# Kernel tuning notes

Hardware: AMD Instinct MI355X
Metric: run time of the kernel (lower is better)

The kernel has to match this reference:

```python
import jax, jax.numpy as jnp
import numpy as np

B, C, O, N, T, K = 4, 64, 64, 32768, 4, 9
PAD, DIL = 4, 1  # padding*dilation, dilation
SIGMA = 0.05
EPS_BN = 1e-5


def _gather_ch(x, idx):
    # x: [B, C, N], idx: [B, N] -> gather along last dim per channel
    idx3 = jnp.broadcast_to(idx[:, None, :], x.shape)
    return jnp.take_along_axis(x, idx3, axis=-1)


def _weighted_conv(x, coords, w):
    # x: [B,C,N], coords: [B,3,N], w: [O,C,K]
    xp = jnp.pad(x, ((0, 0), (0, 0), (PAD, PAD)))
    cp = jnp.pad(coords, ((0, 0), (0, 0), (PAD, PAD)))
    win_idx = jnp.arange(N)[:, None] + jnp.arange(K) * DIL  # [N, K]
    win = xp[:, :, win_idx]   # [B,C,N,K]
    cwin = cp[:, :, win_idx]  # [B,3,N,K]
    d = cwin - cwin[:, :, :, K // 2:K // 2 + 1]
    s = jnp.sum(d * d, axis=1)                    # [B,N,K]
    r = jnp.sqrt(jnp.where(s > 0, s, 1.0))
    r = jnp.where(s > 0, r, 0.0)
    wgt = jnp.maximum(1.0 - r / SIGMA, 0.0)       # [B,N,K]
    return jnp.einsum('bcnk,bnk,ock->bon', win, wgt, w)


def _bn(x, g, b):
    # training-mode BatchNorm1d over (B, N)
    m = jnp.mean(x, axis=(0, 2), keepdims=True)
    v = jnp.var(x, axis=(0, 2), keepdims=True)
    return g[None, :, None] * (x - m) * jax.lax.rsqrt(v + EPS_BN) + b[None, :, None]


def setup_inputs() -> dict:
    key = jax.random.key(0)
    ks = jax.random.split(key, 12)
    inp = jax.random.normal(ks[0], (B, C, N), dtype=jnp.float32)
    # coords in a small box so sigma=0.05 yields non-trivial weights
    multi_coords = jax.random.uniform(ks[1], (B, 3, N, T), dtype=jnp.float32) * 0.02
    indices = jax.random.randint(ks[2], (B, N, T), 0, N, dtype=jnp.int32)
    reindices = jax.random.randint(ks[3], (B, N, T), 0, N, dtype=jnp.int32)
    fan = C * K
    conv_w = jax.random.normal(ks[4], (T, O, C, K), dtype=jnp.float32) / np.sqrt(fan)
    bn_gamma = jnp.ones((T, O), dtype=jnp.float32)
    bn_beta = jnp.zeros((T, O), dtype=jnp.float32)
    fusion_w = jax.random.normal(ks[5], (O, T * O), dtype=jnp.float32) / np.sqrt(T * O)
    fusion_b = jnp.zeros((O,), dtype=jnp.float32)
    fusion_gamma = jnp.ones((O,), dtype=jnp.float32)
    fusion_beta = jnp.zeros((O,), dtype=jnp.float32)
    return {"input": inp, "multi_coords": multi_coords, "indices": indices,
            "reindices": reindices, "conv_w": conv_w, "bn_gamma": bn_gamma,
            "bn_beta": bn_beta, "fusion_w": fusion_w, "fusion_b": fusion_b,
            "fusion_gamma": fusion_gamma, "fusion_beta": fusion_beta}


def reference(input, multi_coords, indices, reindices, conv_w, bn_gamma, bn_beta,
              fusion_w, fusion_b, fusion_gamma, fusion_beta):
    outs = []
    for i in range(T):  # fixed small set of 4 Hilbert orders
        x = _gather_ch(input, indices[:, :, i])            # [B,C,N]
        x = _weighted_conv(x, multi_coords[:, :, :, i], conv_w[i])  # [B,O,N]
        x = _bn(x, bn_gamma[i], bn_beta[i])
        x = _gather_ch(x, reindices[:, :, i])
        outs.append(x)
    cat = jnp.concatenate(outs, axis=1)                    # [B, T*O, N]
    y = jnp.einsum('bcn,oc->bon', cat, fusion_w) + fusion_b[None, :, None]
    y = _bn(y, fusion_gamma, fusion_beta)
    return jax.nn.relu(y)
```

## Files before the change

### kernel.cpp

```cpp
#include <hip/hip_runtime.h>
#include <hip/hip_bf16.h>

#define BB 4
#define CC 64
#define OO 64
#define NN 32768
#define TT 4
#define KK 9
#define PADW 4
#define SIGMA 0.05f
#define EPS_BN 1e-5f

typedef __attribute__((ext_vector_type(8))) short bf16x8;
typedef __attribute__((ext_vector_type(4))) float f32x4;

__device__ __forceinline__ unsigned short f2bf(float f) {
  __hip_bfloat16 h = __float2bfloat16(f);
  return *reinterpret_cast<unsigned short*>(&h);
}
__device__ __forceinline__ unsigned int pkbf(float a, float b) {
  float2 t; t.x = a; t.y = b;
  __hip_bfloat162 h = __float22bfloat162_rn(t);
  unsigned int r;
  __builtin_memcpy(&r, &h, 4);
  return r;
}

__global__ __launch_bounds__(256) void prep_kernel(
    const float* __restrict__ inp, unsigned short* __restrict__ xTb,
    const float* __restrict__ cw,  unsigned short* __restrict__ W4,
    const int*   __restrict__ ind, const float* __restrict__ mc,
    int* __restrict__ indT, float* __restrict__ mcT)
{
  __shared__ float xt[64][65];
  const int bid = blockIdx.x;
  const int tid = threadIdx.x;

  if (bid < 2048) {
    const int n0 = (bid & 511) * 64;
    const int b  = bid >> 9;
    {
      int nl = tid & 63, c4 = tid >> 6;
      #pragma unroll
      for (int i = 0; i < 16; ++i) {
        int c = c4 * 16 + i;
        xt[c][nl] = inp[((size_t)(b*CC + c))*NN + n0 + nl];
      }
    }
    __syncthreads();
    {
      int nl = tid >> 2, cq = tid & 3;
      unsigned int pk[8];
      #pragma unroll
      for (int i = 0; i < 8; ++i) {
        int c = cq*16 + i*2;
        pk[i] = pkbf(xt[c][nl], xt[c+1][nl]);
      }
      unsigned int* dst = (unsigned int*)(xTb + (((size_t)b*NN) + n0 + nl)*CC + cq*16);
      ((int4*)dst)[0] = make_int4((int)pk[0],(int)pk[1],(int)pk[2],(int)pk[3]);
      ((int4*)dst)[1] = make_int4((int)pk[4],(int)pk[5],(int)pk[6],(int)pk[7]);
    }
  } else if (bid < 2560) {
    const int id = bid - 2048;
    const int n  = (id & 127) * 256 + tid;
    const int b  = id >> 7;
    int4 iv = *(const int4*)(ind + ((size_t)b*NN + n)*TT);
    indT[((size_t)(0*BB + b))*NN + n] = iv.x;
    indT[((size_t)(1*BB + b))*NN + n] = iv.y;
    indT[((size_t)(2*BB + b))*NN + n] = iv.z;
    indT[((size_t)(3*BB + b))*NN + n] = iv.w;
    #pragma unroll
    for (int d = 0; d < 3; ++d) {
      float4 mv = *(const float4*)(mc + (((size_t)(b*3 + d))*NN + n)*TT);
      mcT[((size_t)((0*BB + b)*3 + d))*NN + n] = mv.x;
      mcT[((size_t)((1*BB + b)*3 + d))*NN + n] = mv.y;
      mcT[((size_t)((2*BB + b)*3 + d))*NN + n] = mv.z;
      mcT[((size_t)((3*BB + b)*3 + d))*NN + n] = mv.w;
    }
  } else {
    const int id = bid - 2560;
    const int k = id % KK;
    const int t = id / KK;
    for (int u = tid; u < OO*CC; u += 256) {
      int o = u >> 6, c = u & 63;
      int ow = o >> 5, ot = (o >> 4) & 1, l15 = o & 15;
      int frag = c >> 5, q = (c >> 3) & 3, j = c & 7;
      float wv = cw[(((size_t)(t*OO + o))*CC + c)*KK + k];
      W4[(size_t)(t*9+k)*4096 + ow*2048 + ot*1024 + frag*512 + l15*32 + q*8 + j]
          = f2bf(wv);
    }
  }
}

__global__ __launch_bounds__(256, 3) void conv_kernel(
    const unsigned short* __restrict__ xTb,
    const float* __restrict__ mcT,
    const int*   __restrict__ indT,
    const unsigned short* __restrict__ W4,
    unsigned short* __restrict__ Y,
    float* __restrict__ cpart2)
{
  const int n0  = blockIdx.x * 256;
  const int b   = blockIdx.y;
  const int t   = blockIdx.z;
  const int tid = threadIdx.x;
  const int lane = tid & 63;
  const int w    = tid >> 6;
  const int l15  = lane & 15;
  const int q    = lane >> 4;
  const int ow   = w & 1;
  const int nw   = w >> 1;

  __shared__ short xg[264*64];
  __shared__ float wgl[256][10];
  __shared__ float mcs[3][268];
  __shared__ int   ids[268];

  for (int u = tid; u < 264; u += 256) {
    int m = n0 + u - PADW;
    bool v = (m >= 0) && (m < NN);
    ids[u] = v ? indT[((size_t)(t*BB + b))*NN + m] : -1;
    #pragma unroll
    for (int d = 0; d < 3; ++d)
      mcs[d][u] = v ? mcT[((size_t)((t*BB + b)*3 + d))*NN + m] : 0.f;
  }
  __syncthreads();

  int4 g[9];
  #pragma unroll
  for (int i = 0; i < 9; ++i) {
    int u = tid + 256*i;
    g[i] = make_int4(0,0,0,0);
    if (u < 2112) {
      int p = u >> 3, s = u & 7;
      int idx = ids[p];
      if (idx >= 0)
        g[i] = *(const int4*)(xTb + ((size_t)b*NN + idx)*CC + s*8);
    }
  }

  {
    int nl = tid;
    float cx = mcs[0][nl+4], cy = mcs[1][nl+4], cz = mcs[2][nl+4];
    #pragma unroll
    for (int k = 0; k < KK; ++k) {
      float dx = mcs[0][nl+k]-cx, dy = mcs[1][nl+k]-cy, dz = mcs[2][nl+k]-cz;
      float s2 = dx*dx + dy*dy + dz*dz;
      float r = (s2 > 0.f) ? sqrtf(s2) : 0.f;
      wgl[nl][k] = fmaxf(1.f - r*(1.f/SIGMA), 0.f);
    }
  }

  #pragma unroll
  for (int i = 0; i < 9; ++i) {
    int u = tid + 256*i;
    if (u < 2112) {
      int p = u >> 3, s = u & 7;
      *(int4*)&xg[(p << 6) + ((s ^ (p & 7)) << 3)] = g[i];
    }
  }
  __syncthreads();

  const unsigned short* Wt = W4 + (size_t)t*9*4096 + ow*2048 + (l15*4 + q)*8;
  const f32x4 Z = {0.f, 0.f, 0.f, 0.f};
  f32x4 fin[2][8];
  #pragma unroll
  for (int ot = 0; ot < 2; ++ot)
    #pragma unroll
    for (int ns = 0; ns < 8; ++ns) fin[ot][ns] = Z;

  for (int k = 0; k < KK; ++k) {
    const unsigned short* Wk = Wt + (size_t)k*4096;
    bf16x8 af[2][2];
    #pragma unroll
    for (int ot = 0; ot < 2; ++ot) {
      af[ot][0] = *(const bf16x8*)(Wk + ot*1024);
      af[ot][1] = *(const bf16x8*)(Wk + ot*1024 + 512);
    }
    #pragma unroll
    for (int ns = 0; ns < 8; ++ns) {
      int nl = nw*128 + ns*16 + l15;
      int p  = nl + k;
      const short* row = &xg[p << 6];
      int sw = p & 7;
      bf16x8 b0 = *(const bf16x8*)(row + ((q ^ sw) << 3));
      bf16x8 b1 = *(const bf16x8*)(row + (((4 + q) ^ sw) << 3));
      float wgt = wgl[nl][k];
      #pragma unroll
      for (int ot = 0; ot < 2; ++ot) {
        f32x4 d = __builtin_amdgcn_mfma_f32_16x16x32_bf16(af[ot][0], b0, Z, 0, 0, 0);
        d = __builtin_amdgcn_mfma_f32_16x16x32_bf16(af[ot][1], b1, d, 0, 0, 0);
        fin[ot][ns] += wgt * d;
      }
    }
  }

  #pragma unroll
  for (int ns = 0; ns < 8; ++ns) {
    int nl = nw*128 + ns*16 + l15;
    size_t row = (((size_t)t*BB + b)*NN + n0 + nl)*OO;
    #pragma unroll
    for (int ot = 0; ot < 2; ++ot) {
      uint2 pk2;
      pk2.x = pkbf(fin[ot][ns][0], fin[ot][ns][1]);
      pk2.y = pkbf(fin[ot][ns][2], fin[ot][ns][3]);
      *(uint2*)(Y + row + ow*32 + ot*16 + q*4) = pk2;
    }
  }

  float sv[16];
  #pragma unroll
  for (int ot = 0; ot < 2; ++ot)
    #pragma unroll
    for (int r = 0; r < 4; ++r) {
      float a = 0.f, qs = 0.f;
      #pragma unroll
      for (int ns = 0; ns < 8; ++ns) {
        float v = fin[ot][ns][r];
        a += v; qs += v*v;
      }
      sv[ot*4+r] = a; sv[8+ot*4+r] = qs;
    }
  #pragma unroll
  for (int msk = 1; msk < 16; msk <<= 1) {
    #pragma unroll
    for (int i = 0; i < 16; ++i) sv[i] += __shfl_xor(sv[i], msk, 16);
  }
  if (l15 == 0) {
    int slot4 = ((b*128 + (int)blockIdx.x) << 2) | w;
    #pragma unroll
    for (int ot = 0; ot < 2; ++ot)
      #pragma unroll
      for (int r = 0; r < 4; ++r) {
        int o = ow*32 + ot*16 + q*4 + r;
        cpart2[((size_t)((t*64 + o)*2 + 0))*2048 + slot4] = sv[ot*4+r];
        cpart2[((size_t)((t*64 + o)*2 + 1))*2048 + slot4] = sv[8+ot*4+r];
      }
  }
}

__global__ __launch_bounds__(256) void bnparam_kernel(
    const float* __restrict__ cpart2,
    const float* __restrict__ gam,
    const float* __restrict__ bet,
    float* __restrict__ ss)
{
  const int to = blockIdx.x;
  const int tid = threadIdx.x;
  __shared__ float r1[256], r2[256];
  const float* p1 = cpart2 + (size_t)to*2*2048;
  const float* p2 = p1 + 2048;
  float s1 = 0.f, s2 = 0.f;
  for (int i = tid*4; i < 2048; i += 1024) {
    float4 a = *(const float4*)(p1 + i);
    float4 c = *(const float4*)(p2 + i);
    s1 += a.x + a.y + a.z + a.w;
    s2 += c.x + c.y + c.z + c.w;
  }
  r1[tid] = s1; r2[tid] = s2;
  __syncthreads();
  for (int st = 128; st > 0; st >>= 1) {
    if (tid < st) { r1[tid] += r1[tid+st]; r2[tid] += r2[tid+st]; }
    __syncthreads();
  }
  if (tid == 0) {
    const float inv = 1.f / (float)(BB * NN);
    float mean = r1[0] * inv;
    float var  = r2[0] * inv - mean * mean;
    float sc = gam[to] * rsqrtf(var + EPS_BN);
    ss[to*2 + 0] = sc;
    ss[to*2 + 1] = bet[to] - mean * sc;
  }
}

__global__ __launch_bounds__(256) void wfuse_kernel(
    const float* __restrict__ fw,
    const float* __restrict__ fb,
    const float* __restrict__ ss,
    float* __restrict__ fbp,
    unsigned short* __restrict__ FWB)
{
  const int tid = threadIdx.x;
  {
    int o = tid >> 2, c0 = (tid & 3) * 64;
    float s = 0.f;
    for (int c = c0; c < c0 + 64; ++c)
      s += fw[o*256 + c] * ss[c*2 + 1];
    s += __shfl_xor(s, 1);
    s += __shfl_xor(s, 2);
    if ((tid & 3) == 0) fbp[o] = fb[o] + s;
  }
  for (int e = tid; e < 16384; e += 256) {
    int rk  = e >> 11;
    int ow  = (e >> 10) & 1;
    int ot  = (e >> 9) & 1;
    int l15 = (e >> 5) & 15;
    int cj  = e & 31;
    int o = ow*32 + ot*16 + l15;
    int c = (rk >> 1)*64 + (rk & 1)*32 + cj;
    FWB[e] = f2bf(fw[o*256 + c] * ss[c*2]);
  }
}

__global__ __launch_bounds__(256, 4) void fusion_kernel(
    const unsigned short* __restrict__ Y,
    const int*   __restrict__ rind,
    const unsigned short* __restrict__ FWB,
    const float* __restrict__ fbp,
    float* __restrict__ out,
    float* __restrict__ fpart2)
{
  const int n0  = blockIdx.x * 128;
  const int b   = blockIdx.y;
  const int tid = threadIdx.x;
  const int lane = tid & 63;
  const int w    = tid >> 6;
  const int l15  = lane & 15;
  const int q    = lane >> 4;
  const int ow   = w & 1;
  const int nw   = w >> 1;

  __shared__ short zg[128*64];

  int4 rg[4];
  #pragma unroll
  for (int i = 0; i < 4; ++i) {
    int n = (tid >> 3) + 32*i;
    rg[i] = *(const int4*)(rind + ((size_t)b*NN + n0 + n)*TT);
  }

  f32x4 fin[2][4];
  #pragma unroll
  for (int ot = 0; ot < 2; ++ot)
    #pragma unroll
    for (int ns = 0; ns < 4; ++ns) fin[ot][ns] = (f32x4){0.f,0.f,0.f,0.f};

  #pragma unroll
  for (int r = 0; r < 4; ++r) {
    if (r) __syncthreads();
    #pragma unroll
    for (int i = 0; i < 4; ++i) {
      int u = tid + 256*i;
      int n = u >> 3, s = u & 7;
      int rn = (r == 0) ? rg[i].x : (r == 1) ? rg[i].y
             : (r == 2) ? rg[i].z : rg[i].w;
      int4 raw = *(const int4*)(Y + (((size_t)r*BB + b)*NN + rn)*OO + s*8);
      *(int4*)&zg[(n << 6) + ((s ^ (n & 7)) << 3)] = raw;
    }
    __syncthreads();

    #pragma unroll
    for (int kk = 0; kk < 2; ++kk) {
      int rk = r*2 + kk;
      const unsigned short* wp = FWB + rk*2048 + ow*1024 + (l15*4 + q)*8;
      bf16x8 af[2];
      af[0] = *(const bf16x8*)(wp);
      af[1] = *(const bf16x8*)(wp + 512);
      #pragma unroll
      for (int ns = 0; ns < 4; ++ns) {
        int nl = nw*64 + ns*16 + l15;
        int ch = (kk*4 + q) ^ (nl & 7);
        bf16x8 bfr = *(const bf16x8*)&zg[(nl << 6) + (ch << 3)];
        #pragma unroll
        for (int ot = 0; ot < 2; ++ot)
          fin[ot][ns] = __builtin_amdgcn_mfma_f32_16x16x32_bf16(af[ot], bfr, fin[ot][ns], 0, 0, 0);
      }
    }
  }

  float sv[16];
  #pragma unroll
  for (int ot = 0; ot < 2; ++ot)
    #pragma unroll
    for (int r2 = 0; r2 < 4; ++r2) {
      int o = ow*32 + ot*16 + q*4 + r2;
      float bias = fbp[o];
      float* dst = out + ((size_t)(b*OO + o))*NN + n0 + nw*64;
      float a = 0.f, qs = 0.f;
      #pragma unroll
      for (int ns = 0; ns < 4; ++ns) {
        float v = fin[ot][ns][r2] + bias;
        dst[ns*16 + l15] = v;
        a += v; qs += v*v;
      }
      sv[ot*4+r2] = a; sv[8+ot*4+r2] = qs;
    }
  #pragma unroll
  for (int msk = 1; msk < 16; msk <<= 1) {
    #pragma unroll
    for (int i = 0; i < 16; ++i) sv[i] += __shfl_xor(sv[i], msk, 16);
  }
  if (l15 == 0) {
    int slot4 = ((b*256 + (int)blockIdx.x) << 2) | w;
    #pragma unroll
    for (int ot = 0; ot < 2; ++ot)
      #pragma unroll
      for (int r2 = 0; r2 < 4; ++r2) {
        int o = ow*32 + ot*16 + q*4 + r2;
        fpart2[((size_t)(o*2 + 0))*4096 + slot4] = sv[ot*4+r2];
        fpart2[((size_t)(o*2 + 1))*4096 + slot4] = sv[8+ot*4+r2];
      }
  }
}

__global__ __launch_bounds__(256) void freduce_kernel(
    const float* __restrict__ fpart2,
    const float* __restrict__ fg,
    const float* __restrict__ fbeta,
    float* __restrict__ fss)
{
  const int o = blockIdx.x;
  const int tid = threadIdx.x;
  __shared__ float r1[256], r2[256];
  const float* p1 = fpart2 + (size_t)o*2*4096;
  const float* p2 = p1 + 4096;
  float s1 = 0.f, s2 = 0.f;
  for (int i = tid*4; i < 4096; i += 1024) {
    float4 a = *(const float4*)(p1 + i);
    float4 c = *(const float4*)(p2 + i);
    s1 += a.x + a.y + a.z + a.w;
    s2 += c.x + c.y + c.z + c.w;
  }
  r1[tid] = s1; r2[tid] = s2;
  __syncthreads();
  for (int st = 128; st > 0; st >>= 1) {
    if (tid < st) { r1[tid] += r1[tid+st]; r2[tid] += r2[tid+st]; }
    __syncthreads();
  }
  if (tid == 0) {
    const float inv = 1.f / (float)(BB * NN);
    float mean = r1[0] * inv;
    float var  = r2[0] * inv - mean * mean;
    float sc = fg[o] * rsqrtf(var + EPS_BN);
    fss[o*2 + 0] = sc;
    fss[o*2 + 1] = fbeta[o] - mean * sc;
  }
}

__global__ __launch_bounds__(256) void final_kernel(
    float* __restrict__ out, const float* __restrict__ fss)
{
  const int e0 = blockIdx.x * 2048 + threadIdx.x;
  #pragma unroll
  for (int s = 0; s < 8; ++s) {
    int e  = e0 + s * 256;
    int o2 = (e >> 15) & 63;
    float sc = fss[o2*2 + 0];
    float sh = fss[o2*2 + 1];
    float v = out[e] * sc + sh;
    out[e] = fmaxf(v, 0.f);
  }
}

extern "C" void kernel_launch(void* const* d_in, const int* in_sizes, int n_in,
                              void* d_out, int out_size, void* d_ws, size_t ws_size,
                              hipStream_t stream) {
  const float* inp  = (const float*)d_in[0];
  const float* mc   = (const float*)d_in[1];
  const int*   ind  = (const int*)  d_in[2];
  const int*   rind = (const int*)  d_in[3];
  const float* cw   = (const float*)d_in[4];
  const float* bg   = (const float*)d_in[5];
  const float* bb   = (const float*)d_in[6];
  const float* fw   = (const float*)d_in[7];
  const float* fb   = (const float*)d_in[8];
  const float* fg   = (const float*)d_in[9];
  const float* fbt  = (const float*)d_in[10];

  char* ws = (char*)d_ws;
  float* convss = (float*)(ws + 0);
  float* fss    = (float*)(ws + 2048);
  float* fbp    = (float*)(ws + 3072);
  unsigned short* Y = (unsigned short*)(ws + 8192);
  float* fpart2 = (float*)(ws + 8192 + 67108864);
  unsigned short* FWB = (unsigned short*)(ws + 8192 + 67108864 + 2097152);

  char* ob = (char*)d_out;
  unsigned short* xTb = (unsigned short*)ob;
  unsigned short* W4  = (unsigned short*)(ob + 16777216);
  float* cpart2 = (float*)(ob + 17072128);
  int*   indT   = (int*)  (ob + 21266432);
  float* mcT    = (float*)(ob + 23363584);
  float* out = (float*)d_out;

  prep_kernel<<<2596, 256, 0, stream>>>(inp, xTb, cw, W4, ind, mc, indT, mcT);

  dim3 gc(NN/256, BB, TT);
  conv_kernel<<<gc, 256, 0, stream>>>(xTb, mcT, indT, W4, Y, cpart2);

  bnparam_kernel<<<256, 256, 0, stream>>>(cpart2, bg, bb, convss);

  wfuse_kernel<<<1, 256, 0, stream>>>(fw, fb, convss, fbp, FWB);

  dim3 gf(NN/128, BB);
  fusion_kernel<<<gf, 256, 0, stream>>>(Y, rind, FWB, fbp, out, fpart2);

  freduce_kernel<<<OO, 256, 0, stream>>>(fpart2, fg, fbt, fss);

  final_kernel<<<(BB*OO*NN)/2048, 256, 0, stream>>>(out, fss);
}
```

Measured before the change: 216.2 us.

## Use direct global-to-LDS loads for gathers in conv and fusion kernels

Replaces the register-staged gather (global load into registers, then swizzled LDS store) in the conv and fusion kernels with global_load_lds 16-byte direct copies. The swizzle moves to the source address, and a zeroed page in workspace stands in for out-of-range rows. The fusion kernel also hoists its weight fragment loads ahead of the barrier, and the final ReLU/BN kernel switches to float4 accesses. This is meant to cut VGPR pressure and LDS write instructions and to overlap gathers with the weight computation, at the cost of relying on the per-wave contiguous LDS layout of global_load_lds.

Measured after the change: 220.6 us. 1.02x slower.

```diff
diff --git a/kernel.cpp b/kernel.cpp
--- a/kernel.cpp
+++ b/kernel.cpp
@@ -25,12 +25,19 @@
   __builtin_memcpy(&r, &h, 4);
   return r;
 }
+__device__ __forceinline__ void gload16(const void* g, void* l) {
+  __builtin_amdgcn_global_load_lds(
+      (const __attribute__((address_space(1))) void*)g,
+      (__attribute__((address_space(3))) void*)l,
+      16, 0, 0);
+}
 
 __global__ __launch_bounds__(256) void prep_kernel(
     const float* __restrict__ inp, unsigned short* __restrict__ xTb,
     const float* __restrict__ cw,  unsigned short* __restrict__ W4,
     const int*   __restrict__ ind, const float* __restrict__ mc,
-    int* __restrict__ indT, float* __restrict__ mcT)
+    int* __restrict__ indT, float* __restrict__ mcT,
+    float* __restrict__ zpage)
 {
   __shared__ float xt[64][65];
   const int bid = blockIdx.x;
@@ -77,7 +84,7 @@
       mcT[((size_t)((2*BB + b)*3 + d))*NN + n] = mv.z;
       mcT[((size_t)((3*BB + b)*3 + d))*NN + n] = mv.w;
     }
-  } else {
+  } else if (bid < 2596) {
     const int id = bid - 2560;
     const int k = id % KK;
     const int t = id / KK;
@@ -89,6 +96,8 @@
       W4[(size_t)(t*9+k)*4096 + ow*2048 + ot*1024 + frag*512 + l15*32 + q*8 + j]
           = f2bf(wv);
     }
+  } else {
+    zpage[tid] = 0.f;
   }
 }
 
@@ -97,6 +106,7 @@
     const float* __restrict__ mcT,
     const int*   __restrict__ indT,
     const unsigned short* __restrict__ W4,
+    const float* __restrict__ zpage,
     unsigned short* __restrict__ Y,
     float* __restrict__ cpart2)
 {
@@ -126,16 +136,18 @@
   }
   __syncthreads();
 
-  int4 g[9];
   #pragma unroll
   for (int i = 0; i < 9; ++i) {
-    int u = tid + 256*i;
-    g[i] = make_int4(0,0,0,0);
-    if (u < 2112) {
-      int p = u >> 3, s = u & 7;
+    int chunk = w + 4*i;
+    if (chunk < 33) {
+      int u = chunk*64 + lane;
+      int p = u >> 3, c = u & 7;
       int idx = ids[p];
-      if (idx >= 0)
-        g[i] = *(const int4*)(xTb + ((size_t)b*NN + idx)*CC + s*8);
+      int sg = c ^ (p & 7);
+      const void* src = (idx >= 0)
+          ? (const void*)(xTb + ((size_t)b*NN + idx)*CC + sg*8)
+          : (const void*)((const unsigned short*)zpage + c*8);
+      gload16(src, &xg[chunk*512]);
     }
   }
 
@@ -148,15 +160,6 @@
       float s2 = dx*dx + dy*dy + dz*dz;
       float r = (s2 > 0.f) ? sqrtf(s2) : 0.f;
       wgl[nl][k] = fmaxf(1.f - r*(1.f/SIGMA), 0.f);
-    }
-  }
-
-  #pragma unroll
-  for (int i = 0; i < 9; ++i) {
-    int u = tid + 256*i;
-    if (u < 2112) {
-      int p = u >> 3, s = u & 7;
-      *(int4*)&xg[(p << 6) + ((s ^ (p & 7)) << 3)] = g[i];
     }
   }
   __syncthreads();
@@ -340,22 +343,25 @@
     if (r) __syncthreads();
     #pragma unroll
     for (int i = 0; i < 4; ++i) {
-      int u = tid + 256*i;
-      int n = u >> 3, s = u & 7;
+      int chunk = w + 4*i;
+      int u = chunk*64 + lane;
+      int n = u >> 3, c = u & 7;
       int rn = (r == 0) ? rg[i].x : (r == 1) ? rg[i].y
              : (r == 2) ? rg[i].z : rg[i].w;
-      int4 raw = *(const int4*)(Y + (((size_t)r*BB + b)*NN + rn)*OO + s*8);
-      *(int4*)&zg[(n << 6) + ((s ^ (n & 7)) << 3)] = raw;
+      int sg = c ^ (n & 7);
+      gload16(Y + (((size_t)r*BB + b)*NN + rn)*OO + sg*8, &zg[chunk*512]);
+    }
+    bf16x8 af[2][2];
+    #pragma unroll
+    for (int kk = 0; kk < 2; ++kk) {
+      const unsigned short* wp = FWB + (r*2+kk)*2048 + ow*1024 + (l15*4 + q)*8;
+      af[kk][0] = *(const bf16x8*)(wp);
+      af[kk][1] = *(const bf16x8*)(wp + 512);
     }
     __syncthreads();
 
     #pragma unroll
     for (int kk = 0; kk < 2; ++kk) {
-      int rk = r*2 + kk;
-      const unsigned short* wp = FWB + rk*2048 + ow*1024 + (l15*4 + q)*8;
-      bf16x8 af[2];
-      af[0] = *(const bf16x8*)(wp);
-      af[1] = *(const bf16x8*)(wp + 512);
       #pragma unroll
       for (int ns = 0; ns < 4; ++ns) {
         int nl = nw*64 + ns*16 + l15;
@@ -363,7 +369,7 @@
         bf16x8 bfr = *(const bf16x8*)&zg[(nl << 6) + (ch << 3)];
         #pragma unroll
         for (int ot = 0; ot < 2; ++ot)
-          fin[ot][ns] = __builtin_amdgcn_mfma_f32_16x16x32_bf16(af[ot], bfr, fin[ot][ns], 0, 0, 0);
+          fin[ot][ns] = __builtin_amdgcn_mfma_f32_16x16x32_bf16(af[kk][ot], bfr, fin[ot][ns], 0, 0, 0);
       }
     }
   }
@@ -440,15 +446,19 @@
 __global__ __launch_bounds__(256) void final_kernel(
     float* __restrict__ out, const float* __restrict__ fss)
 {
-  const int e0 = blockIdx.x * 2048 + threadIdx.x;
-  #pragma unroll
-  for (int s = 0; s < 8; ++s) {
-    int e  = e0 + s * 256;
+  const int base = blockIdx.x * 2048 + threadIdx.x * 4;
+  #pragma unroll
+  for (int s = 0; s < 2; ++s) {
+    int e = base + s * 1024;
     int o2 = (e >> 15) & 63;
     float sc = fss[o2*2 + 0];
     float sh = fss[o2*2 + 1];
-    float v = out[e] * sc + sh;
-    out[e] = fmaxf(v, 0.f);
+    float4 v = *(float4*)(out + e);
+    v.x = fmaxf(v.x*sc + sh, 0.f);
+    v.y = fmaxf(v.y*sc + sh, 0.f);
+    v.z = fmaxf(v.z*sc + sh, 0.f);
+    v.w = fmaxf(v.w*sc + sh, 0.f);
+    *(float4*)(out + e) = v;
   }
 }
 
@@ -471,6 +481,7 @@
   float* convss = (float*)(ws + 0);
   float* fss    = (float*)(ws + 2048);
   float* fbp    = (float*)(ws + 3072);
+  float* zpage  = (float*)(ws + 4096);
   unsigned short* Y = (unsigned short*)(ws + 8192);
   float* fpart2 = (float*)(ws + 8192 + 67108864);
   unsigned short* FWB = (unsigned short*)(ws + 8192 + 67108864 + 2097152);
@@ -483,10 +494,10 @@
   float* mcT    = (float*)(ob + 23363584);
   float* out = (float*)d_out;
 
-  prep_kernel<<<2596, 256, 0, stream>>>(inp, xTb, cw, W4, ind, mc, indT, mcT);
+  prep_kernel<<<2597, 256, 0, stream>>>(inp, xTb, cw, W4, ind, mc, indT, mcT, zpage);
 
   dim3 gc(NN/256, BB, TT);
-  conv_kernel<<<gc, 256, 0, stream>>>(xTb, mcT, indT, W4, Y, cpart2);
+  conv_kernel<<<gc, 256, 0, stream>>>(xTb, mcT, indT, W4, zpage, Y, cpart2);
 
   bnparam_kernel<<<256, 256, 0, stream>>>(cpart2, bg, bb, convss);
 
```

## Remap conv and fusion blocks so each batch stays on one XCD pair; vectorize final pass

Applied to the files above, without the earlier changes.

Conv and fusion kernels now use a flat 1D grid. Each block's batch index comes from blockIdx modulo 8, so on MI355X's round-robin XCD dispatch all blocks of one batch land on the same two XCDs and share that XCD's L2 for the gathered xTb or Y data of that batch. The final BN/ReLU pass also switches from scalar accesses to float4 loads and stores. The mapping assumes the hardware dispatch order; if the scheduler does not follow it, locality is unchanged and only the index arithmetic is added.

New measurement: 213.1 us. No clear change (-1.4%).

```diff
diff --git a/kernel.cpp b/kernel.cpp
--- a/kernel.cpp
+++ b/kernel.cpp
@@ -100,9 +100,13 @@
     unsigned short* __restrict__ Y,
     float* __restrict__ cpart2)
 {
-  const int n0  = blockIdx.x * 256;
-  const int b   = blockIdx.y;
-  const int t   = blockIdx.z;
+  const int flat = blockIdx.x;
+  const int xcd  = flat & 7;
+  const int b    = xcd >> 1;
+  const int sub  = (xcd & 1) + 2*(flat >> 3);
+  const int t    = sub >> 7;
+  const int x    = sub & 127;
+  const int n0   = x * 256;
   const int tid = threadIdx.x;
   const int lane = tid & 63;
   const int w    = tid >> 6;
@@ -227,7 +231,7 @@
     for (int i = 0; i < 16; ++i) sv[i] += __shfl_xor(sv[i], msk, 16);
   }
   if (l15 == 0) {
-    int slot4 = ((b*128 + (int)blockIdx.x) << 2) | w;
+    int slot4 = ((b*128 + x) << 2) | w;
     #pragma unroll
     for (int ot = 0; ot < 2; ++ot)
       #pragma unroll
@@ -310,8 +314,11 @@
     float* __restrict__ out,
     float* __restrict__ fpart2)
 {
-  const int n0  = blockIdx.x * 128;
-  const int b   = blockIdx.y;
+  const int flat = blockIdx.x;
+  const int xcd  = flat & 7;
+  const int b    = xcd >> 1;
+  const int x    = (xcd & 1) + 2*(flat >> 3);
+  const int n0   = x * 128;
   const int tid = threadIdx.x;
   const int lane = tid & 63;
   const int w    = tid >> 6;
@@ -391,7 +398,7 @@
     for (int i = 0; i < 16; ++i) sv[i] += __shfl_xor(sv[i], msk, 16);
   }
   if (l15 == 0) {
-    int slot4 = ((b*256 + (int)blockIdx.x) << 2) | w;
+    int slot4 = ((b*256 + x) << 2) | w;
     #pragma unroll
     for (int ot = 0; ot < 2; ++ot)
       #pragma unroll
@@ -440,15 +447,19 @@
 __global__ __launch_bounds__(256) void final_kernel(
     float* __restrict__ out, const float* __restrict__ fss)
 {
-  const int e0 = blockIdx.x * 2048 + threadIdx.x;
-  #pragma unroll
-  for (int s = 0; s < 8; ++s) {
-    int e  = e0 + s * 256;
+  const int base = blockIdx.x * 2048 + threadIdx.x * 4;
+  #pragma unroll
+  for (int s = 0; s < 2; ++s) {
+    int e = base + s * 1024;
     int o2 = (e >> 15) & 63;
     float sc = fss[o2*2 + 0];
     float sh = fss[o2*2 + 1];
-    float v = out[e] * sc + sh;
-    out[e] = fmaxf(v, 0.f);
+    float4 v = *(float4*)(out + e);
+    v.x = fmaxf(v.x*sc + sh, 0.f);
+    v.y = fmaxf(v.y*sc + sh, 0.f);
+    v.z = fmaxf(v.z*sc + sh, 0.f);
+    v.w = fmaxf(v.w*sc + sh, 0.f);
+    *(float4*)(out + e) = v;
   }
 }
 
@@ -485,15 +496,13 @@
 
   prep_kernel<<<2596, 256, 0, stream>>>(inp, xTb, cw, W4, ind, mc, indT, mcT);
 
-  dim3 gc(NN/256, BB, TT);
-  conv_kernel<<<gc, 256, 0, stream>>>(xTb, mcT, indT, W4, Y, cpart2);
+  conv_kernel<<<2048, 256, 0, stream>>>(xTb, mcT, indT, W4, Y, cpart2);
 
   bnparam_kernel<<<256, 256, 0, stream>>>(cpart2, bg, bb, convss);
 
   wfuse_kernel<<<1, 256, 0, stream>>>(fw, fb, convss, fbp, FWB);
 
-  dim3 gf(NN/128, BB);
-  fusion_kernel<<<gf, 256, 0, stream>>>(Y, rind, FWB, fbp, out, fpart2);
+  fusion_kernel<<<1024, 256, 0, stream>>>(Y, rind, FWB, fbp, out, fpart2);
 
   freduce_kernel<<<OO, 256, 0, stream>>>(fpart2, fg, fbt, fss);
 
```
